# Kernel optimization log

Measured on AMD Instinct MI355X. Metric: run time of the kernel, lower is better.

Reference implementation:

```python
import jax, jax.numpy as jnp
import numpy as np


def setup_inputs() -> dict:
    key = jax.random.key(0)
    k1, k2 = jax.random.split(key)
    N, C, T, K = 8192, 3, 2048, 10
    Xt = jax.random.normal(k1, (N, C, T), dtype=jnp.float32)
    y_true = jax.random.randint(k2, (N,), 0, K, dtype=jnp.int64)
    return {"Xt": Xt, "y_true": y_true, "num_classes": K}


def reference(Xt, y_true, num_classes):
    # Within-Class Sum of Squares: for each class k,
    #   loss_k = mean((Xk - mean(Xk, axis=0))**2)  (mean over all elements)
    # total = mean over classes. Assumes all num_classes labels are present
    # (matches torch.unique iteration under this data distribution).
    N = Xt.shape[0]
    D = Xt.shape[1] * Xt.shape[2]  # elements per sample
    sums = jax.ops.segment_sum(Xt, y_true, num_segments=num_classes)        # [K, C, T]
    counts = jax.ops.segment_sum(jnp.ones((N,), Xt.dtype), y_true,
                                 num_segments=num_classes)                  # [K]
    means = sums / counts[:, None, None]                                    # [K, C, T]
    sq = jnp.square(Xt - means[y_true])                                     # [N, C, T]
    sq_per_sample = sq.reshape(N, -1).sum(axis=1)                           # [N]
    sq_sums = jax.ops.segment_sum(sq_per_sample, y_true,
                                  num_segments=num_classes)                 # [K]
    per_class_mse = sq_sums / (counts * D)                                  # [K]
    return per_class_mse.mean()
```

## Files before the change

### kernel.cpp

```cpp
#include <hip/hip_runtime.h>

#define N_SAMP 8192
#define D_DIM 6144
#define K_CLS 10
#define CHUNK 32
#define NWIN (N_SAMP / CHUNK)
#define COLS_PER_BLOCK 1024
#define NGROUPS (D_DIM / COLS_PER_BLOCK)
#define NBLK (NGROUPS * NWIN)
#define PIPE 8

typedef float f4 __attribute__((ext_vector_type(4)));

__device__ inline void atom_add_dev(float* p, float v) {
    __hip_atomic_fetch_add(p, v, __ATOMIC_RELAXED, __HIP_MEMORY_SCOPE_AGENT);
}
__device__ inline float load_dev(const float* p) {
    return __hip_atomic_load(p, __ATOMIC_RELAXED, __HIP_MEMORY_SCOPE_AGENT);
}

__global__ __launch_bounds__(1024) void build_sort(const int* __restrict__ y,
                                                   int* __restrict__ counts,
                                                   int* __restrict__ sorted,
                                                   float* __restrict__ S1,
                                                   float* __restrict__ s2sum,
                                                   unsigned* __restrict__ ctr) {
    __shared__ int M[K_CLS * 1024];
    __shared__ int wsum[16];
    const int tid = threadIdx.x;
    const int lane = tid & 63;
    const int wid = tid >> 6;

    {
        f4 z = {0.f, 0.f, 0.f, 0.f};
        f4* p = (f4*)S1;
#pragma unroll
        for (int i = 0; i < (K_CLS * D_DIM) / (4 * 1024); ++i)
            p[i * 1024 + tid] = z;
        if (tid < K_CLS) s2sum[tid] = 0.f;
        if (tid == K_CLS) *ctr = 0u;
    }

    const int base = tid * 8;
    const int4 ya = ((const int4*)y)[tid * 2];
    const int4 yb = ((const int4*)y)[tid * 2 + 1];
    int yy[8] = {ya.x, ya.y, ya.z, ya.w, yb.x, yb.y, yb.z, yb.w};
    int h[K_CLS];
#pragma unroll
    for (int k = 0; k < K_CLS; ++k) h[k] = 0;
#pragma unroll
    for (int i = 0; i < 8; ++i)
#pragma unroll
        for (int k = 0; k < K_CLS; ++k) h[k] += (yy[i] == k) ? 1 : 0;
#pragma unroll
    for (int k = 0; k < K_CLS; ++k) M[k * 1024 + tid] = h[k];
    __syncthreads();

    int loc[K_CLS];
    int run = 0;
#pragma unroll
    for (int j = 0; j < K_CLS; ++j) { loc[j] = run; run += M[tid * K_CLS + j]; }
    int v = run;
#pragma unroll
    for (int d = 1; d < 64; d <<= 1) {
        int n = __shfl_up(v, d, 64);
        if (lane >= d) v += n;
    }
    if (lane == 63) wsum[wid] = v;
    __syncthreads();
    int wbase = 0;
#pragma unroll
    for (int w = 0; w < 16; ++w) wbase += (w < wid) ? wsum[w] : 0;
    const int tbase = wbase + (v - run);
    __syncthreads();
#pragma unroll
    for (int j = 0; j < K_CLS; ++j) M[tid * K_CLS + j] = tbase + loc[j];
    __syncthreads();

    if (tid < K_CLS) {
        const int s = M[tid * 1024];
        const int e = (tid == K_CLS - 1) ? N_SAMP : M[(tid + 1) * 1024];
        counts[tid] = e - s;
    }

    int off[K_CLS];
#pragma unroll
    for (int k = 0; k < K_CLS; ++k) off[k] = M[k * 1024 + tid];
#pragma unroll
    for (int i = 0; i < 8; ++i)
#pragma unroll
        for (int k = 0; k < K_CLS; ++k)
            if (yy[i] == k) sorted[off[k]++] = (k << 16) | (base + i);
}

__global__ __launch_bounds__(256) void wcss_accum(const float* __restrict__ X,
                                                  const int* __restrict__ sorted,
                                                  const int* __restrict__ counts,
                                                  float* __restrict__ S1,
                                                  float* __restrict__ s2sum,
                                                  unsigned* __restrict__ ctr,
                                                  float* __restrict__ out) {
    __shared__ int off_lds[CHUNK];
    __shared__ int cls_lds[CHUNK];
    __shared__ float wred[4];
    __shared__ int last_s;
    const int tid = threadIdx.x;
    const int lane = tid & 63;
    const int wid = tid >> 6;
    const int col0 = blockIdx.x * COLS_PER_BLOCK + tid * 4;

    if (tid < CHUNK) {
        const int p = sorted[blockIdx.y * CHUNK + tid];
        off_lds[tid] = (p & 0xffff) * (D_DIM * (int)sizeof(float));
        cls_lds[tid] = p >> 16;
    }
    __syncthreads();

    const char* basep = (const char*)(X + col0);
    f4 a1 = {0.f, 0.f, 0.f, 0.f};
    float s2c = 0.f;
    int kcur = __builtin_amdgcn_readfirstlane(cls_lds[0]);

    f4 buf[PIPE];
#pragma unroll
    for (int j = 0; j < PIPE; ++j)
        buf[j] = *(const f4*)(basep + (size_t)off_lds[j]);

#pragma unroll
    for (int s = 0; s < CHUNK; ++s) {
        const f4 v = buf[s & (PIPE - 1)];
        if (s + PIPE < CHUNK)
            buf[s & (PIPE - 1)] =
                *(const f4*)(basep + (size_t)off_lds[s + PIPE]);

        const int yk = __builtin_amdgcn_readfirstlane(cls_lds[s]);
        if (yk != kcur) {
            float* b1 = S1 + kcur * D_DIM + col0;
            atom_add_dev(b1 + 0, a1.x); atom_add_dev(b1 + 1, a1.y);
            atom_add_dev(b1 + 2, a1.z); atom_add_dev(b1 + 3, a1.w);
            float r = s2c;
#pragma unroll
            for (int o = 32; o > 0; o >>= 1) r += __shfl_down(r, o, 64);
            if (lane == 0) wred[wid] = r;
            __syncthreads();
            if (tid == 0)
                atom_add_dev(&s2sum[kcur],
                             wred[0] + wred[1] + wred[2] + wred[3]);
            __syncthreads();
            a1 = (f4){0.f, 0.f, 0.f, 0.f};
            s2c = 0.f;
            kcur = yk;
        }
        a1 += v;
        s2c += v.x * v.x + v.y * v.y + v.z * v.z + v.w * v.w;
    }

    float* b1 = S1 + kcur * D_DIM + col0;
    atom_add_dev(b1 + 0, a1.x); atom_add_dev(b1 + 1, a1.y);
    atom_add_dev(b1 + 2, a1.z); atom_add_dev(b1 + 3, a1.w);
#pragma unroll
    for (int o = 32; o > 0; o >>= 1) s2c += __shfl_down(s2c, o, 64);
    if (lane == 0) wred[wid] = s2c;
    asm volatile("s_waitcnt vmcnt(0)" ::: "memory");
    __syncthreads();
    if (tid == 0) {
        atom_add_dev(&s2sum[kcur], wred[0] + wred[1] + wred[2] + wred[3]);
        asm volatile("s_waitcnt vmcnt(0)" ::: "memory");
        unsigned t = __hip_atomic_fetch_add(ctr, 1u, __ATOMIC_RELAXED,
                                            __HIP_MEMORY_SCOPE_AGENT);
        last_s = (t == (unsigned)(NBLK - 1)) ? 1 : 0;
    }
    __syncthreads();
    if (!last_s) return;

    float part = 0.f;
#pragma unroll
    for (int k = 0; k < K_CLS; ++k) {
        const float c = (float)counts[k];
        const float inv2 = 1.0f / (c * c * (float)D_DIM * (float)K_CLS);
        const float* Sk = S1 + k * D_DIM;
        for (int j = 0; j < D_DIM / 256; ++j) {
            float vv = load_dev(&Sk[j * 256 + tid]);
            part -= vv * vv * inv2;
        }
        if (tid == 0)
            part += load_dev(&s2sum[k]) / (c * (float)D_DIM * (float)K_CLS);
    }
    float r = part;
#pragma unroll
    for (int o = 32; o > 0; o >>= 1) r += __shfl_down(r, o, 64);
    if (lane == 0) wred[wid] = r;
    __syncthreads();
    if (tid == 0) *out = wred[0] + wred[1] + wred[2] + wred[3];
}

extern "C" void kernel_launch(void* const* d_in, const int* in_sizes, int n_in,
                              void* d_out, int out_size, void* d_ws, size_t ws_size,
                              hipStream_t stream) {
    const float* X = (const float*)d_in[0];
    const int* y = (const int*)d_in[1];

    float* S1 = (float*)d_ws;
    float* s2sum = S1 + K_CLS * D_DIM;
    int* counts = (int*)(s2sum + K_CLS);
    int* sorted = counts + K_CLS;
    unsigned* ctr = (unsigned*)(sorted + N_SAMP);
    float* out = (float*)d_out;

    build_sort<<<dim3(1), dim3(1024), 0, stream>>>(y, counts, sorted,
                                                   S1, s2sum, ctr);
    wcss_accum<<<dim3(NGROUPS, NWIN), dim3(256), 0, stream>>>(X, sorted, counts,
                                                              S1, s2sum, ctr, out);
}
```

Measured before the change: 301.0 us.

## Replace block-wide s2 reduction with per-wave atomics and unroll row pipeline

At each class boundary, the block-wide reduction through LDS with two __syncthreads is replaced by a per-wave shuffle reduction followed by one atomic per wave. This removes barriers from the streaming loop. The row loop is manually unrolled into eight named register buffers, row offsets are made wave-uniform via readfirstlane, and launch bounds now request 6 blocks per CU. Each boundary now issues four times as many s2sum atomics, and the occupancy hint may push the compiler to limit registers.

```diff
diff --git a/kernel.cpp b/kernel.cpp
--- a/kernel.cpp
+++ b/kernel.cpp
@@ -12,11 +12,16 @@
 
 typedef float f4 __attribute__((ext_vector_type(4)));
 
-__device__ inline void atom_add_dev(float* p, float v) {
+__device__ __forceinline__ void atom_add_dev(float* p, float v) {
     __hip_atomic_fetch_add(p, v, __ATOMIC_RELAXED, __HIP_MEMORY_SCOPE_AGENT);
 }
-__device__ inline float load_dev(const float* p) {
+__device__ __forceinline__ float load_dev(const float* p) {
     return __hip_atomic_load(p, __ATOMIC_RELAXED, __HIP_MEMORY_SCOPE_AGENT);
+}
+__device__ __forceinline__ float wave_sum(float x) {
+#pragma unroll
+    for (int o = 32; o > 0; o >>= 1) x += __shfl_down(x, o, 64);
+    return x;
 }
 
 __global__ __launch_bounds__(1024) void build_sort(const int* __restrict__ y,
@@ -93,13 +98,13 @@
             if (yy[i] == k) sorted[off[k]++] = (k << 16) | (base + i);
 }
 
-__global__ __launch_bounds__(256) void wcss_accum(const float* __restrict__ X,
-                                                  const int* __restrict__ sorted,
-                                                  const int* __restrict__ counts,
-                                                  float* __restrict__ S1,
-                                                  float* __restrict__ s2sum,
-                                                  unsigned* __restrict__ ctr,
-                                                  float* __restrict__ out) {
+__global__ __launch_bounds__(256, 6) void wcss_accum(const float* __restrict__ X,
+                                                     const int* __restrict__ sorted,
+                                                     const int* __restrict__ counts,
+                                                     float* __restrict__ S1,
+                                                     float* __restrict__ s2sum,
+                                                     unsigned* __restrict__ ctr,
+                                                     float* __restrict__ out) {
     __shared__ int off_lds[CHUNK];
     __shared__ int cls_lds[CHUNK];
     __shared__ float wred[4];
@@ -121,51 +126,51 @@
     float s2c = 0.f;
     int kcur = __builtin_amdgcn_readfirstlane(cls_lds[0]);
 
-    f4 buf[PIPE];
-#pragma unroll
-    for (int j = 0; j < PIPE; ++j)
-        buf[j] = *(const f4*)(basep + (size_t)off_lds[j]);
-
-#pragma unroll
-    for (int s = 0; s < CHUNK; ++s) {
-        const f4 v = buf[s & (PIPE - 1)];
-        if (s + PIPE < CHUNK)
-            buf[s & (PIPE - 1)] =
-                *(const f4*)(basep + (size_t)off_lds[s + PIPE]);
-
-        const int yk = __builtin_amdgcn_readfirstlane(cls_lds[s]);
-        if (yk != kcur) {
-            float* b1 = S1 + kcur * D_DIM + col0;
-            atom_add_dev(b1 + 0, a1.x); atom_add_dev(b1 + 1, a1.y);
-            atom_add_dev(b1 + 2, a1.z); atom_add_dev(b1 + 3, a1.w);
-            float r = s2c;
-#pragma unroll
-            for (int o = 32; o > 0; o >>= 1) r += __shfl_down(r, o, 64);
-            if (lane == 0) wred[wid] = r;
-            __syncthreads();
-            if (tid == 0)
-                atom_add_dev(&s2sum[kcur],
-                             wred[0] + wred[1] + wred[2] + wred[3]);
-            __syncthreads();
-            a1 = (f4){0.f, 0.f, 0.f, 0.f};
-            s2c = 0.f;
-            kcur = yk;
-        }
-        a1 += v;
-        s2c += v.x * v.x + v.y * v.y + v.z * v.z + v.w * v.w;
-    }
-
-    float* b1 = S1 + kcur * D_DIM + col0;
-    atom_add_dev(b1 + 0, a1.x); atom_add_dev(b1 + 1, a1.y);
-    atom_add_dev(b1 + 2, a1.z); atom_add_dev(b1 + 3, a1.w);
-#pragma unroll
-    for (int o = 32; o > 0; o >>= 1) s2c += __shfl_down(s2c, o, 64);
-    if (lane == 0) wred[wid] = s2c;
+#define LOADROW(r) (*(const f4*)(basep + \
+        (size_t)__builtin_amdgcn_readfirstlane(off_lds[(r)])))
+
+    f4 q0 = LOADROW(0), q1 = LOADROW(1), q2 = LOADROW(2), q3 = LOADROW(3);
+    f4 q4 = LOADROW(4), q5 = LOADROW(5), q6 = LOADROW(6), q7 = LOADROW(7);
+
+#define STEP(S, Q)                                                          \
+    {                                                                       \
+        const f4 v = Q;                                                     \
+        if ((S) + PIPE < CHUNK) Q = LOADROW((S) + PIPE);                    \
+        const int yk = __builtin_amdgcn_readfirstlane(cls_lds[(S)]);        \
+        if (yk != kcur) {            \
+            float* p1 = S1 + kcur * D_DIM + col0;                           \
+            atom_add_dev(p1 + 0, a1.x); atom_add_dev(p1 + 1, a1.y);         \
+            atom_add_dev(p1 + 2, a1.z); atom_add_dev(p1 + 3, a1.w);         \
+            float r_ = wave_sum(s2c);                                       \
+            if (lane == 0) atom_add_dev(&s2sum[kcur], r_);                  \
+            a1 = (f4){0.f, 0.f, 0.f, 0.f};                                  \
+            s2c = 0.f;                                                      \
+            kcur = yk;                                                      \
+        }                                                                   \
+        a1 += v;                                                            \
+        s2c += v.x * v.x + v.y * v.y + v.z * v.z + v.w * v.w;               \
+    }
+
+    STEP(0, q0)  STEP(1, q1)  STEP(2, q2)  STEP(3, q3)
+    STEP(4, q4)  STEP(5, q5)  STEP(6, q6)  STEP(7, q7)
+    STEP(8, q0)  STEP(9, q1)  STEP(10, q2) STEP(11, q3)
+    STEP(12, q4) STEP(13, q5) STEP(14, q6) STEP(15, q7)
+    STEP(16, q0) STEP(17, q1) STEP(18, q2) STEP(19, q3)
+    STEP(20, q4) STEP(21, q5) STEP(22, q6) STEP(23, q7)
+    STEP(24, q0) STEP(25, q1) STEP(26, q2) STEP(27, q3)
+    STEP(28, q4) STEP(29, q5) STEP(30, q6) STEP(31, q7)
+#undef STEP
+#undef LOADROW
+
+    float* p1 = S1 + kcur * D_DIM + col0;
+    atom_add_dev(p1 + 0, a1.x); atom_add_dev(p1 + 1, a1.y);
+    atom_add_dev(p1 + 2, a1.z); atom_add_dev(p1 + 3, a1.w);
+    float rw = wave_sum(s2c);
+    if (lane == 0) atom_add_dev(&s2sum[kcur], rw);
+
     asm volatile("s_waitcnt vmcnt(0)" ::: "memory");
     __syncthreads();
     if (tid == 0) {
-        atom_add_dev(&s2sum[kcur], wred[0] + wred[1] + wred[2] + wred[3]);
-        asm volatile("s_waitcnt vmcnt(0)" ::: "memory");
         unsigned t = __hip_atomic_fetch_add(ctr, 1u, __ATOMIC_RELAXED,
                                             __HIP_MEMORY_SCOPE_AGENT);
         last_s = (t == (unsigned)(NBLK - 1)) ? 1 : 0;
@@ -186,9 +191,7 @@
         if (tid == 0)
             part += load_dev(&s2sum[k]) / (c * (float)D_DIM * (float)K_CLS);
     }
-    float r = part;
-#pragma unroll
-    for (int o = 32; o > 0; o >>= 1) r += __shfl_down(r, o, 64);
+    float r = wave_sum(part);
     if (lane == 0) wred[wid] = r;
     __syncthreads();
     if (tid == 0) *out = wred[0] + wred[1] + wred[2] + wred[3];
```

Result: slower. 336.5 us (+11.8%).
